# Kernel optimization log

Hardware: AMD Instinct MI355X
Metric: run time of the kernel (lower is better)

The kernel has to match this reference:

```python
import jax, jax.numpy as jnp
import numpy as np

N, E = 20000, 160000
H, C1, C_OUT, D_IN = 4, 256, 512, 128
HID = H * C1  # 1024


def gat_conv(x, src, dst, W, a_src, a_dst, b, heads, ch, concat):
    n = x.shape[0]
    xw = (x @ W).reshape(n, heads, ch)                     # [N,H,C]
    es = jnp.sum(xw * a_src, axis=-1)                      # [N,H]
    ed = jnp.sum(xw * a_dst, axis=-1)                      # [N,H]
    e = jax.nn.leaky_relu(es[src] + ed[dst], 0.2)          # [Etot,H]
    m = jax.ops.segment_max(e, dst, num_segments=n)
    m = jnp.where(jnp.isfinite(m), m, 0.0)
    p = jnp.exp(e - m[dst])
    denom = jax.ops.segment_sum(p, dst, num_segments=n)
    alpha = p / (denom[dst] + 1e-16)                       # segment softmax
    out = jax.ops.segment_sum(alpha[:, :, None] * xw[src], dst, num_segments=n)
    out = out.reshape(n, heads * ch) if concat else out.mean(axis=1)
    return out + b


def layer_norm(x, g, b, eps=1e-5):
    mu = jnp.mean(x, axis=-1, keepdims=True)
    var = jnp.var(x, axis=-1, keepdims=True)
    return (x - mu) * jax.lax.rsqrt(var + eps) * g + b


def setup_inputs() -> dict:
    key = jax.random.key(0)
    ks = jax.random.split(key, 16)
    s1, s2, s3 = (2.0 / D_IN) ** 0.5, (2.0 / HID) ** 0.5, (2.0 / HID) ** 0.5
    return {
        "x": jax.random.normal(ks[0], (N, D_IN), jnp.float32),
        "edge_index": jax.random.randint(ks[1], (2, E), 0, N, jnp.int64),
        "W1": jax.random.normal(ks[2], (D_IN, H * C1), jnp.float32) * s1,
        "a_src1": jax.random.normal(ks[3], (H, C1), jnp.float32) * 0.1,
        "a_dst1": jax.random.normal(ks[4], (H, C1), jnp.float32) * 0.1,
        "b1": jnp.zeros((HID,), jnp.float32),
        "ln1_g": jnp.ones((HID,), jnp.float32),
        "ln1_b": jnp.zeros((HID,), jnp.float32),
        "W2": jax.random.normal(ks[5], (HID, H * C1), jnp.float32) * s2,
        "a_src2": jax.random.normal(ks[6], (H, C1), jnp.float32) * 0.1,
        "a_dst2": jax.random.normal(ks[7], (H, C1), jnp.float32) * 0.1,
        "b2": jnp.zeros((HID,), jnp.float32),
        "ln2_g": jnp.ones((HID,), jnp.float32),
        "ln2_b": jnp.zeros((HID,), jnp.float32),
        "W3": jax.random.normal(ks[8], (HID, C_OUT), jnp.float32) * s3,
        "a_src3": jax.random.normal(ks[9], (1, C_OUT), jnp.float32) * 0.1,
        "a_dst3": jax.random.normal(ks[10], (1, C_OUT), jnp.float32) * 0.1,
        "b3": jnp.zeros((C_OUT,), jnp.float32),
    }


def reference(x, edge_index, W1, a_src1, a_dst1, b1, ln1_g, ln1_b,
              W2, a_src2, a_dst2, b2, ln2_g, ln2_b,
              W3, a_src3, a_dst3, b3):
    # add self loops (PyG GATConv default add_self_loops=True)
    loops = jnp.arange(N, dtype=edge_index.dtype)
    src = jnp.concatenate([edge_index[0], loops])
    dst = jnp.concatenate([edge_index[1], loops])

    h = gat_conv(x, src, dst, W1, a_src1, a_dst1, b1, H, C1, True)
    h = jax.nn.elu(layer_norm(h, ln1_g, ln1_b))  # dropout: eval mode (identity)
    h = gat_conv(h, src, dst, W2, a_src2, a_dst2, b2, H, C1, True)
    h = jax.nn.elu(layer_norm(h, ln2_g, ln2_b))
    out = gat_conv(h, src, dst, W3, a_src3, a_dst3, b3, 1, C_OUT, True)
    return out
```

## Files before the change

kernel.cpp:

```cpp
#include <hip/hip_runtime.h>
#include <hip/hip_bf16.h>

typedef __hip_bfloat16 bf16;
typedef __attribute__((ext_vector_type(8))) short short8;
typedef __attribute__((ext_vector_type(4))) float float4v;

#define NN 20000
#define EE 160000
#define ET (NN + EE)

__device__ __forceinline__ float bf2f(bf16 v){ return __bfloat162float(v); }
__device__ __forceinline__ float raw2f(unsigned short u){ return __uint_as_float(((unsigned)u) << 16); }
__device__ __forceinline__ unsigned short f2raw(float f){
  bf16 h = __float2bfloat16(f);
  return *(unsigned short*)&h;
}

__device__ __forceinline__ int detect_f32(const void* raw, int nwords, int lane){
  unsigned v = ((const unsigned*)raw)[lane % nwords];
  int e8 = (v >> 7) & 0xFF;
  int looks = (e8 >= 100 && e8 <= 140) ? 1 : 0;
  unsigned long long mz = __ballot(v == 0u);
  unsigned long long ml = __ballot(looks);
  int nz = __popcll(mz);
  int nonz = 64 - nz;
  int nl = __popcll(ml);
  return (nonz > 0 && 2*nl >= nonz) ? 0 : 1;
}

__device__ __forceinline__ int detect_i64(const int* eiraw, int lane){
  int odd = eiraw[2*lane + 1];
  unsigned long long m2 = __ballot(odd != 0);
  return (m2 == 0ULL) ? 1 : 0;
}

struct P13 { const void* src[13]; int off[13]; int n[13]; };
struct PrepArgs {
  const void* xraw; bf16* Xc;
  const void* w1raw; bf16* Wt1;
  const void* w2raw; bf16* Wt2;
  const void* w3raw; bf16* Wt3;
  const int* eiraw; int* eic;
  P13 p13; float* prm;
  int* counts;
  float* esA; float* edA;
};

__device__ __forceinline__ void do_transpose(float (*tile)[33], const void* raw,
    bf16* wt, int K, int M, int f, int bx, int by, int t){
  int kb = by*32, mb = bx*32;
  int tx = t & 31, ty = t >> 5;
  for (int r = 0; r < 4; r++){
    int k = kb + ty + r*8;
    int m = mb + tx;
    float v = f ? ((const float*)raw)[(size_t)k*M+m] : bf2f(((const bf16*)raw)[(size_t)k*M+m]);
    tile[ty + r*8][tx] = v;
  }
  __syncthreads();
  for (int r = 0; r < 4; r++){
    int m = mb + ty + r*8;
    int k = kb + tx;
    wt[(size_t)m*K + k] = __float2bfloat16(tile[tx][ty + r*8]);
  }
}

__global__ __launch_bounds__(256) void k_prep(PrepArgs A){
  __shared__ float tile[32][33];
  int b = blockIdx.x, t = threadIdx.x;
  int lane = t & 63;
  if (b < 10000){
    int f = detect_f32(A.xraw, NN*128/2, lane);
    int i = b*256 + t;
    if (f) A.Xc[i] = __float2bfloat16(((const float*)A.xraw)[i]);
    else   A.Xc[i] = ((const bf16*)A.xraw)[i];
  } else if (b < 10128){
    int f = detect_f32(A.w1raw, 128*1024/2, lane);
    int r = b - 10000;
    do_transpose(tile, A.w1raw, A.Wt1, 128, 1024, f, r & 31, r >> 5, t);
  } else if (b < 11152){
    int f = detect_f32(A.w2raw, 1024*1024/2, lane);
    int r = b - 10128;
    do_transpose(tile, A.w2raw, A.Wt2, 1024, 1024, f, r & 31, r >> 5, t);
  } else if (b < 11664){
    int f = detect_f32(A.w3raw, 1024*512/2, lane);
    int r = b - 11152;
    do_transpose(tile, A.w3raw, A.Wt3, 1024, 512, f, r & 15, r >> 4, t);
  } else if (b < 12914){
    int f64 = detect_i64(A.eiraw, lane);
    int i = (b - 11664)*256 + t;
    if (i < 2*EE) A.eic[i] = f64 ? A.eiraw[2*i] : A.eiraw[i];
  } else if (b < 12927){
    int pb = b - 12914;
    const void* s = A.p13.src[pb];
    int n = A.p13.n[pb];
    int f = detect_f32(s, n/2, lane);
    float* d = A.prm + A.p13.off[pb];
    for (int i = t; i < n; i += 256)
      d[i] = f ? ((const float*)s)[i] : bf2f(((const bf16*)s)[i]);
  } else if (b < 13006){
    int i = (b - 12927)*256 + t;
    if (i < NN) A.counts[i] = 1;
  } else {
    int i = (b - 13006)*256 + t;
    if (i < NN*4){ A.esA[i] = 0.f; A.edA[i] = 0.f; }
  }
}

__global__ void k_hist(const int* __restrict__ ei, int* __restrict__ counts){
  int e = blockIdx.x*256 + threadIdx.x;
  if (e < EE){
    int d = ei[EE + e];
    if (d >= 0 && d < NN) atomicAdd(&counts[d], 1);
  }
}

__global__ __launch_bounds__(1024) void k_scan(const int* __restrict__ counts, int* __restrict__ rp,
    int* __restrict__ cursor, int* __restrict__ col){
  __shared__ int wsum[16];
  __shared__ int sc;
  int t = threadIdx.x, lane = t & 63, wv = t >> 6;
  if (t == 0) sc = 0;
  __syncthreads();
  for (int base = 0; base < NN; base += 1024){
    int i = base + t;
    int v = (i < NN) ? counts[i] : 0;
    int x = v;
    #pragma unroll
    for (int o = 1; o < 64; o <<= 1){
      int y = __shfl_up(x, o, 64);
      if (lane >= o) x += y;
    }
    if (lane == 63) wsum[wv] = x;
    __syncthreads();
    if (wv == 0 && lane < 16){
      int w = wsum[lane];
      #pragma unroll
      for (int o = 1; o < 16; o <<= 1){
        int y = __shfl_up(w, o, 16);
        if ((lane & 15) >= o) w += y;
      }
      wsum[lane] = w;
    }
    __syncthreads();
    int carry = sc;
    int wpre = (wv > 0) ? wsum[wv-1] : 0;
    if (i < NN){
      int p = carry + wpre + x - v;
      rp[i] = p;
      col[p] = i;
      cursor[i] = p + 1;
    }
    __syncthreads();
    if (t == 1023) sc = carry + wsum[15];
    __syncthreads();
  }
  if (t == 0) rp[NN] = sc;
}

__global__ void k_scatter(const int* __restrict__ ei, int* __restrict__ cursor, int* __restrict__ col){
  int e = blockIdx.x*256 + threadIdx.x;
  if (e < EE){
    int s = ei[e], d = ei[EE + e];
    if (d >= 0 && d < NN){
      int pos = atomicAdd(&cursor[d], 1);
      col[pos] = s;
    }
  }
}

__global__ __launch_bounds__(256) void k_gemm_mfma(
    const bf16* __restrict__ X, const bf16* __restrict__ Wt, bf16* __restrict__ Y,
    const float* __restrict__ as_, const float* __restrict__ ad_,
    float* __restrict__ es, float* __restrict__ ed,
    int K, int M, int C, int H)
{
  __shared__ bf16 Xs[64*64];
  __shared__ bf16 Bs[128*64];
  int ncols = gridDim.x;
  int bid = blockIdx.y * ncols + blockIdx.x;
  int xcd  = bid & 7;
  int rest = bid >> 3;
  int colb = rest % ncols;
  int rowb = xcd + 8 * (rest / ncols);
  int r0 = rowb * 64;
  if (r0 >= NN) return;
  int c0 = colb * 128;

  int tid  = threadIdx.x;
  int wave = tid >> 6, lane = tid & 63;
  int quad = lane >> 4, l15 = lane & 15;
  int wr = (wave >> 1) * 32;
  int wc = (wave & 1) * 64;
  int sw = l15 & 7;

  float4v acc[2][4];
  #pragma unroll
  for (int i=0;i<2;i++)
    #pragma unroll
    for (int j=0;j<4;j++)
      acc[i][j] = (float4v){0.f,0.f,0.f,0.f};

  for (int k0 = 0; k0 < K; k0 += 64){
    #pragma unroll
    for (int i = 0; i < 2; i++){
      int ch = i*256 + tid;
      int row = ch >> 3, kl = ch & 7;
      int kg = kl ^ (row & 7);
      const bf16* gx = X + (size_t)(r0 + row)*K + k0 + kg*8;
      __builtin_amdgcn_global_load_lds(
        (const __attribute__((address_space(1))) unsigned int*)gx,
        (__attribute__((address_space(3))) unsigned int*)(Xs + ch*8), 16, 0, 0);
    }
    #pragma unroll
    for (int i = 0; i < 4; i++){
      int ch = i*256 + tid;
      int row = ch >> 3, kl = ch & 7;
      int kg = kl ^ (row & 7);
      const bf16* gb = Wt + (size_t)(c0 + row)*K + k0 + kg*8;
      __builtin_amdgcn_global_load_lds(
        (const __attribute__((address_space(1))) unsigned int*)gb,
        (__attribute__((address_space(3))) unsigned int*)(Bs + ch*8), 16, 0, 0);
    }
    __syncthreads();

    #pragma unroll
    for (int kk = 0; kk < 2; kk++){
      int kp = quad + kk*4;
      short8 af[2], bfr[4];
      #pragma unroll
      for (int i = 0; i < 2; i++){
        int r = wr + i*16 + l15;
        af[i] = *(const short8*)(Xs + ((size_t)r*8 + (kp ^ sw))*8);
      }
      #pragma unroll
      for (int j = 0; j < 4; j++){
        int r = wc + j*16 + l15;
        bfr[j] = *(const short8*)(Bs + ((size_t)r*8 + (kp ^ sw))*8);
      }
      #pragma unroll
      for (int i = 0; i < 2; i++)
        #pragma unroll
        for (int j = 0; j < 4; j++)
          acc[i][j] = __builtin_amdgcn_mfma_f32_16x16x32_bf16(af[i], bfr[j], acc[i][j], 0, 0, 0);
    }
    __syncthreads();
  }

  int h = c0 / C;
  float asv[4], adv[4];
  #pragma unroll
  for (int j = 0; j < 4; j++){
    int colj = c0 + wc + j*16 + l15;
    asv[j] = as_[colj]; adv[j] = ad_[colj];
  }
  #pragma unroll
  for (int i = 0; i < 2; i++){
    int rbase = r0 + wr + i*16 + quad*4;
    #pragma unroll
    for (int rg = 0; rg < 4; rg++){
      int row = rbase + rg;
      bool ok = (row < NN);
      float pe = 0.f, pd = 0.f;
      #pragma unroll
      for (int j = 0; j < 4; j++){
        float v = acc[i][j][rg];
        int colj = c0 + wc + j*16 + l15;
        if (ok) Y[(size_t)row*M + colj] = __float2bfloat16(v);
        pe += v * asv[j];
        pd += v * adv[j];
      }
      #pragma unroll
      for (int o = 1; o < 16; o <<= 1){
        pe += __shfl_xor(pe, o, 64);
        pd += __shfl_xor(pd, o, 64);
      }
      if (ok && l15 == 0){
        atomicAdd(&es[row*H + h], pe);
        atomicAdd(&ed[row*H + h], pd);
      }
    }
  }
}

__global__ __launch_bounds__(256) void k_aggln(const int* __restrict__ rp, const int* __restrict__ col,
    const bf16* __restrict__ xw, const float* __restrict__ es, const float* __restrict__ ed,
    const float* __restrict__ bias, const float* __restrict__ gam, const float* __restrict__ bet,
    bf16* __restrict__ act, float* __restrict__ esz, float* __restrict__ edz, int zn){
  int wv = threadIdx.x >> 6, lane = threadIdx.x & 63;
  int n = blockIdx.x*4 + wv;
  int h = lane >> 4;
  int cb = lane * 16;
  int e0 = rp[n], e1 = rp[n+1], deg = e1 - e0;
  float4 ed4 = *(const float4*)&ed[n*4];
  const unsigned short* xwu = (const unsigned short*)xw;

  float acc[16];
  #pragma unroll
  for (int c=0;c<16;c++) acc[c]=0.f;

  if (deg <= 64){
    int src = 0;
    float l0=-1e30f, l1=-1e30f, l2=-1e30f, l3=-1e30f;
    if (lane < deg){
      src = col[e0 + lane];
      float4 e4 = *(const float4*)&es[src*4];
      float v;
      v = e4.x + ed4.x; l0 = v > 0.f ? v : 0.2f*v;
      v = e4.y + ed4.y; l1 = v > 0.f ? v : 0.2f*v;
      v = e4.z + ed4.z; l2 = v > 0.f ? v : 0.2f*v;
      v = e4.w + ed4.w; l3 = v > 0.f ? v : 0.2f*v;
    }
    float m0=l0, m1=l1, m2=l2, m3=l3;
    #pragma unroll
    for (int o=1;o<64;o<<=1){
      m0 = fmaxf(m0, __shfl_xor(m0,o,64));
      m1 = fmaxf(m1, __shfl_xor(m1,o,64));
      m2 = fmaxf(m2, __shfl_xor(m2,o,64));
      m3 = fmaxf(m3, __shfl_xor(m3,o,64));
    }
    float p0 = (lane<deg) ? __expf(l0-m0) : 0.f;
    float p1 = (lane<deg) ? __expf(l1-m1) : 0.f;
    float p2 = (lane<deg) ? __expf(l2-m2) : 0.f;
    float p3 = (lane<deg) ? __expf(l3-m3) : 0.f;
    float d0=p0, d1=p1, d2=p2, d3=p3;
    #pragma unroll
    for (int o=1;o<64;o<<=1){
      d0 += __shfl_xor(d0,o,64);
      d1 += __shfl_xor(d1,o,64);
      d2 += __shfl_xor(d2,o,64);
      d3 += __shfl_xor(d3,o,64);
    }
    float al0 = p0 * (1.f/(d0+1e-16f));
    float al1 = p1 * (1.f/(d1+1e-16f));
    float al2 = p2 * (1.f/(d2+1e-16f));
    float al3 = p3 * (1.f/(d3+1e-16f));

    int j = 0;
    for (; j + 2 <= deg; j += 2){
      int sA = __shfl(src, j, 64);
      int sB = __shfl(src, j+1, 64);
      float a0A = __shfl(al0, j, 64), a1A = __shfl(al1, j, 64);
      float a2A = __shfl(al2, j, 64), a3A = __shfl(al3, j, 64);
      float a0B = __shfl(al0, j+1, 64), a1B = __shfl(al1, j+1, 64);
      float a2B = __shfl(al2, j+1, 64), a3B = __shfl(al3, j+1, 64);
      float aA = (h==0) ? a0A : ((h==1) ? a1A : ((h==2) ? a2A : a3A));
      float aB = (h==0) ? a0B : ((h==1) ? a1B : ((h==2) ? a2B : a3B));
      const unsigned short* rA = xwu + (size_t)sA*1024 + cb;
      const unsigned short* rB = xwu + (size_t)sB*1024 + cb;
      ushort4 uA0 = *(const ushort4*)(rA);
      ushort4 uA1 = *(const ushort4*)(rA+4);
      ushort4 uA2 = *(const ushort4*)(rA+8);
      ushort4 uA3 = *(const ushort4*)(rA+12);
      ushort4 uB0 = *(const ushort4*)(rB);
      ushort4 uB1 = *(const ushort4*)(rB+4);
      ushort4 uB2 = *(const ushort4*)(rB+8);
      ushort4 uB3 = *(const ushort4*)(rB+12);
      acc[0] += aA*raw2f(uA0.x); acc[1] += aA*raw2f(uA0.y); acc[2] += aA*raw2f(uA0.z); acc[3] += aA*raw2f(uA0.w);
      acc[4] += aA*raw2f(uA1.x); acc[5] += aA*raw2f(uA1.y); acc[6] += aA*raw2f(uA1.z); acc[7] += aA*raw2f(uA1.w);
      acc[8] += aA*raw2f(uA2.x); acc[9] += aA*raw2f(uA2.y); acc[10]+= aA*raw2f(uA2.z); acc[11]+= aA*raw2f(uA2.w);
      acc[12]+= aA*raw2f(uA3.x); acc[13]+= aA*raw2f(uA3.y); acc[14]+= aA*raw2f(uA3.z); acc[15]+= aA*raw2f(uA3.w);
      acc[0] += aB*raw2f(uB0.x); acc[1] += aB*raw2f(uB0.y); acc[2] += aB*raw2f(uB0.z); acc[3] += aB*raw2f(uB0.w);
      acc[4] += aB*raw2f(uB1.x); acc[5] += aB*raw2f(uB1.y); acc[6] += aB*raw2f(uB1.z); acc[7] += aB*raw2f(uB1.w);
      acc[8] += aB*raw2f(uB2.x); acc[9] += aB*raw2f(uB2.y); acc[10]+= aB*raw2f(uB2.z); acc[11]+= aB*raw2f(uB2.w);
      acc[12]+= aB*raw2f(uB3.x); acc[13]+= aB*raw2f(uB3.y); acc[14]+= aB*raw2f(uB3.z); acc[15]+= aB*raw2f(uB3.w);
    }
    for (; j < deg; j++){
      int s = __shfl(src, j, 64);
      float a0j = __shfl(al0, j, 64);
      float a1j = __shfl(al1, j, 64);
      float a2j = __shfl(al2, j, 64);
      float a3j = __shfl(al3, j, 64);
      float aj = (h==0) ? a0j : ((h==1) ? a1j : ((h==2) ? a2j : a3j));
      const unsigned short* row = xwu + (size_t)s*1024 + cb;
      ushort4 u0 = *(const ushort4*)(row);
      ushort4 u1 = *(const ushort4*)(row+4);
      ushort4 u2 = *(const ushort4*)(row+8);
      ushort4 u3 = *(const ushort4*)(row+12);
      acc[0] += aj*raw2f(u0.x); acc[1] += aj*raw2f(u0.y); acc[2] += aj*raw2f(u0.z); acc[3] += aj*raw2f(u0.w);
      acc[4] += aj*raw2f(u1.x); acc[5] += aj*raw2f(u1.y); acc[6] += aj*raw2f(u1.z); acc[7] += aj*raw2f(u1.w);
      acc[8] += aj*raw2f(u2.x); acc[9] += aj*raw2f(u2.y); acc[10]+= aj*raw2f(u2.z); acc[11]+= aj*raw2f(u2.w);
      acc[12]+= aj*raw2f(u3.x); acc[13]+= aj*raw2f(u3.y); acc[14]+= aj*raw2f(u3.z); acc[15]+= aj*raw2f(u3.w);
    }
  } else {
    float edh = (h==0) ? ed4.x : ((h==1) ? ed4.y : ((h==2) ? ed4.z : ed4.w));
    float m = -1e30f;
    for (int e=e0;e<e1;e++){
      float v = es[col[e]*4 + h] + edh;
      v = v > 0.f ? v : 0.2f*v;
      m = fmaxf(m, v);
    }
    float den = 0.f;
    for (int e=e0;e<e1;e++){
      float v = es[col[e]*4 + h] + edh;
      v = v > 0.f ? v : 0.2f*v;
      den += __expf(v - m);
    }
    float rd = 1.f/(den + 1e-16f);
    for (int e=e0;e<e1;e++){
      int s = col[e];
      float v = es[s*4 + h] + edh;
      v = v > 0.f ? v : 0.2f*v;
      float aj = __expf(v - m) * rd;
      const unsigned short* row = xwu + (size_t)s*1024 + cb;
      ushort4 u0 = *(const ushort4*)(row);
      ushort4 u1 = *(const ushort4*)(row+4);
      ushort4 u2 = *(const ushort4*)(row+8);
      ushort4 u3 = *(const ushort4*)(row+12);
      acc[0] += aj*raw2f(u0.x); acc[1] += aj*raw2f(u0.y); acc[2] += aj*raw2f(u0.z); acc[3] += aj*raw2f(u0.w);
      acc[4] += aj*raw2f(u1.x); acc[5] += aj*raw2f(u1.y); acc[6] += aj*raw2f(u1.z); acc[7] += aj*raw2f(u1.w);
      acc[8] += aj*raw2f(u2.x); acc[9] += aj*raw2f(u2.y); acc[10]+= aj*raw2f(u2.z); acc[11]+= aj*raw2f(u2.w);
      acc[12]+= aj*raw2f(u3.x); acc[13]+= aj*raw2f(u3.y); acc[14]+= aj*raw2f(u3.z); acc[15]+= aj*raw2f(u3.w);
    }
  }

  #pragma unroll
  for (int c=0;c<16;c++) acc[c] += bias[cb+c];
  float s1 = 0.f, s2 = 0.f;
  #pragma unroll
  for (int c=0;c<16;c++){ s1 += acc[c]; s2 += acc[c]*acc[c]; }
  #pragma unroll
  for (int o=1;o<64;o<<=1){
    s1 += __shfl_xor(s1,o,64);
    s2 += __shfl_xor(s2,o,64);
  }
  float mu  = s1 * (1.f/1024.f);
  float var = s2 * (1.f/1024.f) - mu*mu;
  float rstd = rsqrtf(fmaxf(var, 0.f) + 1e-5f);

  ushort4 o4[4];
  #pragma unroll
  for (int q=0;q<4;q++){
    float v0 = (acc[q*4+0]-mu)*rstd*gam[cb+q*4+0] + bet[cb+q*4+0];
    float v1 = (acc[q*4+1]-mu)*rstd*gam[cb+q*4+1] + bet[cb+q*4+1];
    float v2 = (acc[q*4+2]-mu)*rstd*gam[cb+q*4+2] + bet[cb+q*4+2];
    float v3 = (acc[q*4+3]-mu)*rstd*gam[cb+q*4+3] + bet[cb+q*4+3];
    v0 = v0 > 0.f ? v0 : (__expf(v0)-1.f);
    v1 = v1 > 0.f ? v1 : (__expf(v1)-1.f);
    v2 = v2 > 0.f ? v2 : (__expf(v2)-1.f);
    v3 = v3 > 0.f ? v3 : (__expf(v3)-1.f);
    o4[q].x = f2raw(v0); o4[q].y = f2raw(v1); o4[q].z = f2raw(v2); o4[q].w = f2raw(v3);
  }
  unsigned short* dst = (unsigned short*)act + (size_t)n*1024 + cb;
  *(ushort4*)(dst)    = o4[0];
  *(ushort4*)(dst+4)  = o4[1];
  *(ushort4*)(dst+8)  = o4[2];
  *(ushort4*)(dst+12) = o4[3];

  if (lane < zn){ esz[n*zn + lane] = 0.f; edz[n*zn + lane] = 0.f; }
}

__global__ __launch_bounds__(256) void k_agg3(const int* __restrict__ rp, const int* __restrict__ col,
    const bf16* __restrict__ xw, const float* __restrict__ es, const float* __restrict__ ed,
    const float* __restrict__ bias, float* __restrict__ out){
  int wv = threadIdx.x >> 6, lane = threadIdx.x & 63;
  int n = blockIdx.x*4 + wv;
  int cb = lane * 8;
  int e0 = rp[n], e1 = rp[n+1], deg = e1 - e0;
  float edv = ed[n];
  const unsigned short* xwu = (const unsigned short*)xw;

  float acc[8];
  #pragma unroll
  for (int c=0;c<8;c++) acc[c]=0.f;

  if (deg <= 64){
    int src = 0;
    float l = -1e30f;
    if (lane < deg){
      src = col[e0 + lane];
      float v = es[src] + edv;
      l = v > 0.f ? v : 0.2f*v;
    }
    float m = l;
    #pragma unroll
    for (int o=1;o<64;o<<=1) m = fmaxf(m, __shfl_xor(m,o,64));
    float p = (lane<deg) ? __expf(l-m) : 0.f;
    float d = p;
    #pragma unroll
    for (int o=1;o<64;o<<=1) d += __shfl_xor(d,o,64);
    float al = p * (1.f/(d+1e-16f));

    int j = 0;
    for (; j + 2 <= deg; j += 2){
      int sA = __shfl(src, j, 64);
      int sB = __shfl(src, j+1, 64);
      float aA = __shfl(al, j, 64);
      float aB = __shfl(al, j+1, 64);
      const unsigned short* rA = xwu + (size_t)sA*512 + cb;
      const unsigned short* rB = xwu + (size_t)sB*512 + cb;
      ushort4 uA0 = *(const ushort4*)(rA);
      ushort4 uA1 = *(const ushort4*)(rA+4);
      ushort4 uB0 = *(const ushort4*)(rB);
      ushort4 uB1 = *(const ushort4*)(rB+4);
      acc[0] += aA*raw2f(uA0.x); acc[1] += aA*raw2f(uA0.y); acc[2] += aA*raw2f(uA0.z); acc[3] += aA*raw2f(uA0.w);
      acc[4] += aA*raw2f(uA1.x); acc[5] += aA*raw2f(uA1.y); acc[6] += aA*raw2f(uA1.z); acc[7] += aA*raw2f(uA1.w);
      acc[0] += aB*raw2f(uB0.x); acc[1] += aB*raw2f(uB0.y); acc[2] += aB*raw2f(uB0.z); acc[3] += aB*raw2f(uB0.w);
      acc[4] += aB*raw2f(uB1.x); acc[5] += aB*raw2f(uB1.y); acc[6] += aB*raw2f(uB1.z); acc[7] += aB*raw2f(uB1.w);
    }
    for (; j < deg; j++){
      int s = __shfl(src, j, 64);
      float aj = __shfl(al, j, 64);
      const unsigned short* row = xwu + (size_t)s*512 + cb;
      ushort4 u0 = *(const ushort4*)(row);
      ushort4 u1 = *(const ushort4*)(row+4);
      acc[0] += aj*raw2f(u0.x); acc[1] += aj*raw2f(u0.y); acc[2] += aj*raw2f(u0.z); acc[3] += aj*raw2f(u0.w);
      acc[4] += aj*raw2f(u1.x); acc[5] += aj*raw2f(u1.y); acc[6] += aj*raw2f(u1.z); acc[7] += aj*raw2f(u1.w);
    }
  } else {
    float m = -1e30f;
    for (int e=e0;e<e1;e++){
      float v = es[col[e]] + edv;
      v = v > 0.f ? v : 0.2f*v;
      m = fmaxf(m, v);
    }
    float den = 0.f;
    for (int e=e0;e<e1;e++){
      float v = es[col[e]] + edv;
      v = v > 0.f ? v : 0.2f*v;
      den += __expf(v - m);
    }
    float rd = 1.f/(den + 1e-16f);
    for (int e=e0;e<e1;e++){
      int s = col[e];
      float v = es[s] + edv;
      v = v > 0.f ? v : 0.2f*v;
      float aj = __expf(v - m) * rd;
      const unsigned short* row = xwu + (size_t)s*512 + cb;
      ushort4 u0 = *(const ushort4*)(row);
      ushort4 u1 = *(const ushort4*)(row+4);
      acc[0] += aj*raw2f(u0.x); acc[1] += aj*raw2f(u0.y); acc[2] += aj*raw2f(u0.z); acc[3] += aj*raw2f(u0.w);
      acc[4] += aj*raw2f(u1.x); acc[5] += aj*raw2f(u1.y); acc[6] += aj*raw2f(u1.z); acc[7] += aj*raw2f(u1.w);
    }
  }
  float* dst = out + (size_t)n*512 + cb;
  #pragma unroll
  for (int c=0;c<8;c++) dst[c] = acc[c] + bias[cb+c];
}

__global__ void k_wssmall(float* __restrict__ out, float code){
  if (threadIdx.x == 0) out[0] = code;
}

extern "C" void kernel_launch(void* const* d_in, const int* in_sizes, int n_in,
                              void* d_out, int out_size, void* d_ws, size_t ws_size,
                              hipStream_t stream){
  float* out = (float*)d_out;
  char* ws = (char*)d_ws;

  static const int EXP_SZ[18] = {2560000, 320000, 131072, 1024,1024,1024,1024,1024,
                                 1048576, 1024,1024,1024,1024,1024,
                                 524288, 512,512,512};
  if (n_in != 18){ k_wssmall<<<1,64,0,stream>>>(out, 500.0f*301.0f); return; }
  for (int i = 0; i < 18; i++)
    if (in_sizes[i] != EXP_SZ[i]){ k_wssmall<<<1,64,0,stream>>>(out, 500.0f*302.0f); return; }
  if (out_size != NN*512){ k_wssmall<<<1,64,0,stream>>>(out, 500.0f*303.0f); return; }
  const size_t NEED = 93215360;
  if (ws_size < NEED){ k_wssmall<<<1,64,0,stream>>>(out, 500.0f*304.0f); return; }

  bf16* xw    = (bf16*) (ws);
  int*  cnt   = (int*)  (ws);
  bf16* act   = (bf16*) (ws + 40960000);
  int*  cursor= (int*)  (ws + 40960000);
  bf16* Xc    = (bf16*) (ws + 81920000);
  float* esC  = (float*)(ws + 81920000);
  float* edC  = (float*)(ws + 82000000);
  bf16* Wt1   = (bf16*) (ws + 87040000);
  bf16* Wt2   = (bf16*) (ws + 87302144);
  bf16* Wt3   = (bf16*) (ws + 89399296);
  float* prm  = (float*)(ws + 90447872);
  int*  eic   = (int*)  (ws + 90495232);
  float* esB  = (float*)(ws + 90495232);
  float* edB  = (float*)(ws + 90815232);
  float* esA  = (float*)(ws + 91775232);
  float* edA  = (float*)(ws + 92095232);
  int*  rp    = (int*)  (ws + 92415232);
  int*  col   = (int*)  (ws + 92495360);

  float *as1=prm+0, *ad1=prm+1024, *b1=prm+2048, *lg1=prm+3072, *lb1=prm+4096;
  float *as2=prm+5120, *ad2=prm+6144, *b2=prm+7168, *lg2=prm+8192, *lb2=prm+9216;
  float *as3=prm+10240, *ad3=prm+10752, *b3=prm+11264;

  const int TB = 256;
  int gbE = (EE + TB - 1)/TB;

  {
    PrepArgs A;
    A.xraw = d_in[0]; A.Xc = Xc;
    A.w1raw = d_in[2]; A.Wt1 = Wt1;
    A.w2raw = d_in[8]; A.Wt2 = Wt2;
    A.w3raw = d_in[14]; A.Wt3 = Wt3;
    A.eiraw = (const int*)d_in[1]; A.eic = eic;
    const int idx[13] = {3,4,5,6,7, 9,10,11,12,13, 15,16,17};
    const int off[13] = {0,1024,2048,3072,4096, 5120,6144,7168,8192,9216, 10240,10752,11264};
    const int nn [13] = {1024,1024,1024,1024,1024, 1024,1024,1024,1024,1024, 512,512,512};
    for (int i=0;i<13;i++){ A.p13.src[i]=d_in[idx[i]]; A.p13.off[i]=off[i]; A.p13.n[i]=nn[i]; }
    A.prm = prm; A.counts = cnt; A.esA = esA; A.edA = edA;
    k_prep<<<13006 + 313, TB, 0, stream>>>(A);
  }

  k_hist<<<gbE, TB, 0, stream>>>(eic, cnt);
  k_scan<<<1, 1024, 0, stream>>>(cnt, rp, cursor, col);
  k_scatter<<<gbE, TB, 0, stream>>>(eic, cursor, col);

  const int RB = (NN + 63)/64;
  const int R8 = ((RB + 7)/8)*8;
  dim3 g12(1024/128, R8);
  dim3 g3 (512/128,  R8);

  k_gemm_mfma<<<g12, TB, 0, stream>>>(Xc, Wt1, xw, as1, ad1, esA, edA, 128, 1024, 256, 4);
  k_aggln<<<NN/4, TB, 0, stream>>>(rp, col, xw, esA, edA, b1, lg1, lb1, act, esB, edB, 4);

  k_gemm_mfma<<<g12, TB, 0, stream>>>(act, Wt2, xw, as2, ad2, esB, edB, 1024, 1024, 256, 4);
  k_aggln<<<NN/4, TB, 0, stream>>>(rp, col, xw, esB, edB, b2, lg2, lb2, act, esC, edC, 1);

  k_gemm_mfma<<<g3, TB, 0, stream>>>(act, Wt3, xw, as3, ad3, esC, edC, 1024, 512, 512, 1);
  k_agg3<<<NN/4, TB, 0, stream>>>(rp, col, xw, esC, edC, b3, out);
}
```

Baseline: 451.9 us.

## Double-buffer LDS tiles in MFMA GEMM to overlap loads with compute

Splits the GEMM tile staging and MFMA compute into helpers and adds a second pair of LDS buffers, so the next K-slice is loaded asynchronously while the current one is multiplied. This aims to hide global-to-LDS latency and halve the number of barriers per K step. It doubles LDS usage per block (48KB), which may reduce occupancy. It also relies on the barrier placement being correct for the ping-pong buffers.

```diff
diff --git a/kernel.cpp b/kernel.cpp
--- a/kernel.cpp
+++ b/kernel.cpp
@@ -168,14 +168,64 @@
   }
 }
 
+__device__ __forceinline__ void stage_tiles(const bf16* __restrict__ X, const bf16* __restrict__ Wt,
+    bf16* xs, bf16* bs, int r0, int c0, int K, int tid, int k0){
+  #pragma unroll
+  for (int i = 0; i < 2; i++){
+    int ch = i*256 + tid;
+    int row = ch >> 3, kl = ch & 7;
+    int kg = kl ^ (row & 7);
+    const bf16* gx = X + (size_t)(r0 + row)*K + k0 + kg*8;
+    __builtin_amdgcn_global_load_lds(
+      (const __attribute__((address_space(1))) unsigned int*)gx,
+      (__attribute__((address_space(3))) unsigned int*)(xs + ch*8), 16, 0, 0);
+  }
+  #pragma unroll
+  for (int i = 0; i < 4; i++){
+    int ch = i*256 + tid;
+    int row = ch >> 3, kl = ch & 7;
+    int kg = kl ^ (row & 7);
+    const bf16* gb = Wt + (size_t)(c0 + row)*K + k0 + kg*8;
+    __builtin_amdgcn_global_load_lds(
+      (const __attribute__((address_space(1))) unsigned int*)gb,
+      (__attribute__((address_space(3))) unsigned int*)(bs + ch*8), 16, 0, 0);
+  }
+}
+
+__device__ __forceinline__ void compute_step(const bf16* xb, const bf16* bb,
+    int wr, int wc, int quad, int l15, int sw, float4v (&acc)[2][4]){
+  #pragma unroll
+  for (int kk = 0; kk < 2; kk++){
+    int kp = quad + kk*4;
+    short8 af[2], bfr[4];
+    #pragma unroll
+    for (int i = 0; i < 2; i++){
+      int r = wr + i*16 + l15;
+      af[i] = *(const short8*)(xb + ((size_t)r*8 + (kp ^ sw))*8);
+    }
+    #pragma unroll
+    for (int j = 0; j < 4; j++){
+      int r = wc + j*16 + l15;
+      bfr[j] = *(const short8*)(bb + ((size_t)r*8 + (kp ^ sw))*8);
+    }
+    #pragma unroll
+    for (int i = 0; i < 2; i++)
+      #pragma unroll
+      for (int j = 0; j < 4; j++)
+        acc[i][j] = __builtin_amdgcn_mfma_f32_16x16x32_bf16(af[i], bfr[j], acc[i][j], 0, 0, 0);
+  }
+}
+
 __global__ __launch_bounds__(256) void k_gemm_mfma(
     const bf16* __restrict__ X, const bf16* __restrict__ Wt, bf16* __restrict__ Y,
     const float* __restrict__ as_, const float* __restrict__ ad_,
     float* __restrict__ es, float* __restrict__ ed,
     int K, int M, int C, int H)
 {
-  __shared__ bf16 Xs[64*64];
-  __shared__ bf16 Bs[128*64];
+  __shared__ bf16 Xs0[64*64];
+  __shared__ bf16 Xs1[64*64];
+  __shared__ bf16 Bs0[128*64];
+  __shared__ bf16 Bs1[128*64];
   int ncols = gridDim.x;
   int bid = blockIdx.y * ncols + blockIdx.x;
   int xcd  = bid & 7;
@@ -200,50 +250,18 @@
     for (int j=0;j<4;j++)
       acc[i][j] = (float4v){0.f,0.f,0.f,0.f};
 
-  for (int k0 = 0; k0 < K; k0 += 64){
-    #pragma unroll
-    for (int i = 0; i < 2; i++){
-      int ch = i*256 + tid;
-      int row = ch >> 3, kl = ch & 7;
-      int kg = kl ^ (row & 7);
-      const bf16* gx = X + (size_t)(r0 + row)*K + k0 + kg*8;
-      __builtin_amdgcn_global_load_lds(
-        (const __attribute__((address_space(1))) unsigned int*)gx,
-        (__attribute__((address_space(3))) unsigned int*)(Xs + ch*8), 16, 0, 0);
-    }
-    #pragma unroll
-    for (int i = 0; i < 4; i++){
-      int ch = i*256 + tid;
-      int row = ch >> 3, kl = ch & 7;
-      int kg = kl ^ (row & 7);
-      const bf16* gb = Wt + (size_t)(c0 + row)*K + k0 + kg*8;
-      __builtin_amdgcn_global_load_lds(
-        (const __attribute__((address_space(1))) unsigned int*)gb,
-        (__attribute__((address_space(3))) unsigned int*)(Bs + ch*8), 16, 0, 0);
-    }
+  int nst = K >> 6;
+  stage_tiles(X, Wt, Xs0, Bs0, r0, c0, K, tid, 0);
+  __syncthreads();
+
+  for (int t = 0; t < nst; t += 2){
+    if (t + 1 < nst) stage_tiles(X, Wt, Xs1, Bs1, r0, c0, K, tid, (t+1) << 6);
+    compute_step(Xs0, Bs0, wr, wc, quad, l15, sw, acc);
     __syncthreads();
-
-    #pragma unroll
-    for (int kk = 0; kk < 2; kk++){
-      int kp = quad + kk*4;
-      short8 af[2], bfr[4];
-      #pragma unroll
-      for (int i = 0; i < 2; i++){
-        int r = wr + i*16 + l15;
-        af[i] = *(const short8*)(Xs + ((size_t)r*8 + (kp ^ sw))*8);
-      }
-      #pragma unroll
-      for (int j = 0; j < 4; j++){
-        int r = wc + j*16 + l15;
-        bfr[j] = *(const short8*)(Bs + ((size_t)r*8 + (kp ^ sw))*8);
-      }
-      #pragma unroll
-      for (int i = 0; i < 2; i++)
-        #pragma unroll
-        for (int j = 0; j < 4; j++)
-          acc[i][j] = __builtin_amdgcn_mfma_f32_16x16x32_bf16(af[i], bfr[j], acc[i][j], 0, 0, 0);
-    }
-    __syncthreads();
+    if (t + 1 >= nst) break;
+    if (t + 2 < nst) stage_tiles(X, Wt, Xs0, Bs0, r0, c0, K, tid, (t+2) << 6);
+    compute_step(Xs1, Bs1, wr, wc, quad, l15, sw, acc);
+    if (t + 2 < nst) __syncthreads();
   }
 
   int h = c0 / C;
```

New measurement: 460.1 us. No clear change (+1.8%).
